# Kernel optimization log

Hardware: AMD Instinct MI355X
Metric: run time of the kernel (lower is better)

## Reference

```python
import jax, jax.numpy as jnp
import numpy as np
import math

NUM_HEADS = 2


def setup_inputs() -> dict:
    key = jax.random.key(0)
    k1, k2, k3, k4 = jax.random.split(key, 4)
    B, S, E = 16, 2048, 8  # embed_dim == n_wires == 8 (required by module structure)
    x = jax.random.normal(k1, (B, S, E), dtype=jnp.float32)
    theta = jax.random.normal(k2, (E,), dtype=jnp.float32)          # trainable RX angles, one per wire
    w_out = jax.random.normal(k3, (E, E), dtype=jnp.float32) / math.sqrt(E)  # out_proj weight
    b_out = jax.random.normal(k4, (E,), dtype=jnp.float32) * 0.01   # out_proj bias
    return {"x": x, "theta": theta, "w_out": w_out, "b_out": b_out}


def reference(x, theta, w_out, b_out):
    B, S, E = x.shape
    H = NUM_HEADS
    dk = E // H
    # Quantum projection, analytic form: per-wire RX(x) then RX(theta) on |0>,
    # PauliZ expectation -> cos(x + theta). Same layer applied for q, k, v.
    q = jnp.cos(x + theta)              # [B, S, E]
    qh = q.reshape(B, S, H, dk).transpose(0, 2, 1, 3)  # [B, H, S, dk]; q == k == v
    scores = jnp.einsum('bhqd,bhkd->bhqk', qh, qh) / jnp.sqrt(jnp.float32(dk))
    attn = jax.nn.softmax(scores, axis=-1)             # dropout is identity in eval
    out = jnp.einsum('bhqk,bhkd->bhqd', attn, qh)      # [B, H, S, dk]
    out = out.transpose(0, 2, 1, 3).reshape(B, S, E)
    return out @ w_out.T + b_out
```

## Files before the change

### kernel.cpp

```cpp
#include <hip/hip_runtime.h>
#include <math.h>

#define BB 16
#define SS 2048
#define HH 2
#define ROWS_PER_BLOCK 128
#define ROWS_PER_WAVE 32
#define THREADS1 256
#define NIH 2
#define KEYS_HALF (SS / NIH)
#define KT 16
#define NITER (KEYS_HALF / KT)
#define KVT_STRIDE 1040

typedef _Float16 half8 __attribute__((ext_vector_type(8)));
typedef _Float16 half4h __attribute__((ext_vector_type(4)));
typedef float floatx4 __attribute__((ext_vector_type(4)));

__device__ __forceinline__ float fast_exp2(float x) {
  return __builtin_amdgcn_exp2f(x);
}

__global__ __launch_bounds__(THREADS1, 4)
void qattn_mfma(const float* __restrict__ x,
                const float* __restrict__ theta,
                float* __restrict__ ws) {
  __shared__ half8 s_keys[KEYS_HALF];
  __shared__ _Float16 s_kvT[5 * KVT_STRIDE];
  __shared__ half4h s_rows[ROWS_PER_BLOCK];

  const int bid = blockIdx.x;
  const int rb  = bid & 15;
  const int bh  = (bid >> 4) & 31;
  const int ih  = bid >> 9;
  const int b   = bh >> 1;
  const int h   = bh & 1;
  const int t   = threadIdx.x;

  const float4 th = ((const float4*)theta)[h];
  const float4* xb = (const float4*)x;

  for (int i = t; i < KEYS_HALF; i += THREADS1) {
    const int s = ih * KEYS_HALF + i;
    float4 xr = xb[(size_t)(b * SS + s) * 2 + h];
    _Float16 c0 = (_Float16)__cosf(xr.x + th.x);
    _Float16 c1 = (_Float16)__cosf(xr.y + th.y);
    _Float16 c2 = (_Float16)__cosf(xr.z + th.z);
    _Float16 c3 = (_Float16)__cosf(xr.w + th.w);
    const _Float16 z = (_Float16)0.0f;
    half8 v = {c0, c1, c2, c3, z, z, z, z};
    s_keys[i] = v;
    s_kvT[0 * KVT_STRIDE + i] = c0;
    s_kvT[1 * KVT_STRIDE + i] = c1;
    s_kvT[2 * KVT_STRIDE + i] = c2;
    s_kvT[3 * KVT_STRIDE + i] = c3;
  }
  for (int i = t; i < KVT_STRIDE; i += THREADS1)
    s_kvT[4 * KVT_STRIDE + i] = (_Float16)1.0f;
  for (int i = t; i < ROWS_PER_BLOCK; i += THREADS1) {
    const int s = rb * ROWS_PER_BLOCK + i;
    float4 xr = xb[(size_t)(b * SS + s) * 2 + h];
    half4h v = {(_Float16)__cosf(xr.x + th.x), (_Float16)__cosf(xr.y + th.y),
                (_Float16)__cosf(xr.z + th.z), (_Float16)__cosf(xr.w + th.w)};
    s_rows[i] = v;
  }
  __syncthreads();

  const int lane = t & 63;
  const int wv   = t >> 6;
  const int quad = lane >> 4;
  const int l15  = lane & 15;

  const float KS  = 0.72134752044448170367f;
  const float scl = (lane < 16) ? KS : 0.0f;
  half4h r0 = s_rows[wv * ROWS_PER_WAVE + l15];
  half4h r1 = s_rows[wv * ROWS_PER_WAVE + 16 + l15];
  const _Float16 z = (_Float16)0.0f;
  half8 b0 = {(_Float16)((float)r0[0] * scl), (_Float16)((float)r0[1] * scl),
              (_Float16)((float)r0[2] * scl), (_Float16)((float)r0[3] * scl), z, z, z, z};
  half8 b1 = {(_Float16)((float)r1[0] * scl), (_Float16)((float)r1[1] * scl),
              (_Float16)((float)r1[2] * scl), (_Float16)((float)r1[3] * scl), z, z, z, z};

  const _Float16* bpv_base =
      s_kvT + (l15 < 4 ? l15 : 4) * KVT_STRIDE + quad * 4;

  floatx4 o0 = {0.f, 0.f, 0.f, 0.f};
  floatx4 o1 = {0.f, 0.f, 0.f, 0.f};
  const floatx4 zf = {0.f, 0.f, 0.f, 0.f};
  half8 apv0 = {z, z, z, z, z, z, z, z};
  half8 apv1 = {z, z, z, z, z, z, z, z};

#pragma unroll 2
  for (int it = 0; it < NITER; ++it) {
    half8 a = s_keys[it * KT + l15];
    half4h bl = *(const half4h*)(bpv_base + it * KT);
    half8 bpv = {bl[0], bl[1], bl[2], bl[3], z, z, z, z};

    floatx4 c0 = __builtin_amdgcn_mfma_f32_16x16x32_f16(a, b0, zf, 0, 0, 0);
    floatx4 c1 = __builtin_amdgcn_mfma_f32_16x16x32_f16(a, b1, zf, 0, 0, 0);

    apv0[0] = (_Float16)fast_exp2(c0[0]);
    apv0[1] = (_Float16)fast_exp2(c0[1]);
    apv0[2] = (_Float16)fast_exp2(c0[2]);
    apv0[3] = (_Float16)fast_exp2(c0[3]);
    apv1[0] = (_Float16)fast_exp2(c1[0]);
    apv1[1] = (_Float16)fast_exp2(c1[1]);
    apv1[2] = (_Float16)fast_exp2(c1[2]);
    apv1[3] = (_Float16)fast_exp2(c1[3]);

    o0 = __builtin_amdgcn_mfma_f32_16x16x32_f16(apv0, bpv, o0, 0, 0, 0);
    o1 = __builtin_amdgcn_mfma_f32_16x16x32_f16(apv1, bpv, o1, 0, 0, 0);
  }

  if (l15 < 5) {
    const size_t base =
        ((size_t)(ih * 32 + bh) * SS + rb * ROWS_PER_BLOCK + wv * ROWS_PER_WAVE) * 8;
    float* w0 = ws + base + (size_t)(quad * 4) * 8 + l15;
    float* w1 = ws + base + (size_t)(16 + quad * 4) * 8 + l15;
    w0[0]  = o0[0]; w0[8]  = o0[1]; w0[16] = o0[2]; w0[24] = o0[3];
    w1[0]  = o1[0]; w1[8]  = o1[1]; w1[16] = o1[2]; w1[24] = o1[3];
  }
}

__global__ __launch_bounds__(256)
void qattn_proj(const float* __restrict__ ws,
                const float* __restrict__ w_out,
                const float* __restrict__ b_out,
                float* __restrict__ out) {
  const int gid = blockIdx.x * 256 + threadIdx.x;
  const int b = gid >> 11;
  const int s = gid & 2047;
  float o[8];
#pragma unroll
  for (int h = 0; h < HH; ++h) {
    const int bh = b * 2 + h;
    const size_t i0 = ((size_t)(0 * 32 + bh) * SS + s) * 8;
    const size_t i1 = ((size_t)(1 * 32 + bh) * SS + s) * 8;
    float4 A  = *(const float4*)(ws + i0);
    float  la = ws[i0 + 4];
    float4 Bv = *(const float4*)(ws + i1);
    float  lb = ws[i1 + 4];
    const float inv = 1.0f / (la + lb);
    o[h * 4 + 0] = (A.x + Bv.x) * inv;
    o[h * 4 + 1] = (A.y + Bv.y) * inv;
    o[h * 4 + 2] = (A.z + Bv.z) * inv;
    o[h * 4 + 3] = (A.w + Bv.w) * inv;
  }
  float r[8];
#pragma unroll
  for (int e = 0; e < 8; ++e) {
    float acc = b_out[e];
#pragma unroll
    for (int j = 0; j < 8; ++j) acc = fmaf(o[j], w_out[e * 8 + j], acc);
    r[e] = acc;
  }
  float* op = out + (size_t)gid * 8;
  *(float4*)op = make_float4(r[0], r[1], r[2], r[3]);
  *(float4*)(op + 4) = make_float4(r[4], r[5], r[6], r[7]);
}

extern "C" void kernel_launch(void* const* d_in, const int* in_sizes, int n_in,
                              void* d_out, int out_size, void* d_ws, size_t ws_size,
                              hipStream_t stream) {
  const float* x     = (const float*)d_in[0];
  const float* theta = (const float*)d_in[1];
  const float* w_out = (const float*)d_in[2];
  const float* b_out = (const float*)d_in[3];
  float* out = (float*)d_out;
  (void)in_sizes; (void)n_in; (void)out_size; (void)ws_size;

  qattn_mfma<<<dim3(NIH * 32 * 16), THREADS1, 0, stream>>>(x, theta, (float*)d_ws);
  qattn_proj<<<dim3((BB * SS) / 256), 256, 0, stream>>>((const float*)d_ws, w_out, b_out, out);
}
```

Before: 80.55 us.

## Fuse attention and output projection into one kernel with atomic head accumulation

Replaces the split-key attention kernel plus separate projection kernel with one fused kernel. Each block now covers all 2048 keys for one head and 128 query rows, using 8 waves of 16 rows each. It normalizes in shared memory and atomically adds each head's partial projection into the output, which is zeroed by a memset. The goal is to drop the workspace round trip and the second launch. In exchange it adds a memset, float atomics, more LDS per block and half as many blocks.

Measured after the change: 80.15 us. Within noise of the previous version (-0.5%).

```diff
diff --git a/kernel.cpp b/kernel.cpp
--- a/kernel.cpp
+++ b/kernel.cpp
@@ -5,43 +5,52 @@
 #define SS 2048
 #define HH 2
 #define ROWS_PER_BLOCK 128
-#define ROWS_PER_WAVE 32
-#define THREADS1 256
-#define NIH 2
-#define KEYS_HALF (SS / NIH)
+#define THREADS1 512
 #define KT 16
-#define NITER (KEYS_HALF / KT)
-#define KVT_STRIDE 1040
+#define NITER (SS / KT)
+#define KVT_STRIDE 2064
 
 typedef _Float16 half8 __attribute__((ext_vector_type(8)));
 typedef _Float16 half4h __attribute__((ext_vector_type(4)));
+typedef _Float16 half2h __attribute__((ext_vector_type(2)));
 typedef float floatx4 __attribute__((ext_vector_type(4)));
 
 __device__ __forceinline__ float fast_exp2(float x) {
   return __builtin_amdgcn_exp2f(x);
 }
 
+__device__ __forceinline__ half2h pkrtz(float a, float b) {
+#if defined(__has_builtin)
+#if __has_builtin(__builtin_amdgcn_cvt_pkrtz)
+  return __builtin_bit_cast(half2h, __builtin_amdgcn_cvt_pkrtz(a, b));
+#else
+  half2h r; r[0] = (_Float16)a; r[1] = (_Float16)b; return r;
+#endif
+#else
+  half2h r; r[0] = (_Float16)a; r[1] = (_Float16)b; return r;
+#endif
+}
+
 __global__ __launch_bounds__(THREADS1, 4)
-void qattn_mfma(const float* __restrict__ x,
-                const float* __restrict__ theta,
-                float* __restrict__ ws) {
-  __shared__ half8 s_keys[KEYS_HALF];
+void qattn_fused(const float* __restrict__ x,
+                 const float* __restrict__ theta,
+                 const float* __restrict__ w_out,
+                 const float* __restrict__ b_out,
+                 float* __restrict__ out) {
+  __shared__ half8 s_keys[SS];
   __shared__ _Float16 s_kvT[5 * KVT_STRIDE];
-  __shared__ half4h s_rows[ROWS_PER_BLOCK];
+  __shared__ float po[ROWS_PER_BLOCK * 6];
 
   const int bid = blockIdx.x;
   const int rb  = bid & 15;
-  const int bh  = (bid >> 4) & 31;
-  const int ih  = bid >> 9;
-  const int b   = bh >> 1;
-  const int h   = bh & 1;
+  const int h   = (bid >> 4) & 1;
+  const int b   = bid >> 5;
   const int t   = threadIdx.x;
 
   const float4 th = ((const float4*)theta)[h];
   const float4* xb = (const float4*)x;
 
-  for (int i = t; i < KEYS_HALF; i += THREADS1) {
-    const int s = ih * KEYS_HALF + i;
+  for (int s = t; s < SS; s += THREADS1) {
     float4 xr = xb[(size_t)(b * SS + s) * 2 + h];
     _Float16 c0 = (_Float16)__cosf(xr.x + th.x);
     _Float16 c1 = (_Float16)__cosf(xr.y + th.y);
@@ -49,21 +58,14 @@
     _Float16 c3 = (_Float16)__cosf(xr.w + th.w);
     const _Float16 z = (_Float16)0.0f;
     half8 v = {c0, c1, c2, c3, z, z, z, z};
-    s_keys[i] = v;
-    s_kvT[0 * KVT_STRIDE + i] = c0;
-    s_kvT[1 * KVT_STRIDE + i] = c1;
-    s_kvT[2 * KVT_STRIDE + i] = c2;
-    s_kvT[3 * KVT_STRIDE + i] = c3;
+    s_keys[s] = v;
+    s_kvT[0 * KVT_STRIDE + s] = c0;
+    s_kvT[1 * KVT_STRIDE + s] = c1;
+    s_kvT[2 * KVT_STRIDE + s] = c2;
+    s_kvT[3 * KVT_STRIDE + s] = c3;
   }
   for (int i = t; i < KVT_STRIDE; i += THREADS1)
     s_kvT[4 * KVT_STRIDE + i] = (_Float16)1.0f;
-  for (int i = t; i < ROWS_PER_BLOCK; i += THREADS1) {
-    const int s = rb * ROWS_PER_BLOCK + i;
-    float4 xr = xb[(size_t)(b * SS + s) * 2 + h];
-    half4h v = {(_Float16)__cosf(xr.x + th.x), (_Float16)__cosf(xr.y + th.y),
-                (_Float16)__cosf(xr.z + th.z), (_Float16)__cosf(xr.w + th.w)};
-    s_rows[i] = v;
-  }
   __syncthreads();
 
   const int lane = t & 63;
@@ -73,90 +75,58 @@
 
   const float KS  = 0.72134752044448170367f;
   const float scl = (lane < 16) ? KS : 0.0f;
-  half4h r0 = s_rows[wv * ROWS_PER_WAVE + l15];
-  half4h r1 = s_rows[wv * ROWS_PER_WAVE + 16 + l15];
+  const int   qrow = rb * ROWS_PER_BLOCK + wv * 16 + l15;
+  half4h rq = *(const half4h*)&s_keys[qrow];
   const _Float16 z = (_Float16)0.0f;
-  half8 b0 = {(_Float16)((float)r0[0] * scl), (_Float16)((float)r0[1] * scl),
-              (_Float16)((float)r0[2] * scl), (_Float16)((float)r0[3] * scl), z, z, z, z};
-  half8 b1 = {(_Float16)((float)r1[0] * scl), (_Float16)((float)r1[1] * scl),
-              (_Float16)((float)r1[2] * scl), (_Float16)((float)r1[3] * scl), z, z, z, z};
+  half8 bq = {(_Float16)((float)rq[0] * scl), (_Float16)((float)rq[1] * scl),
+              (_Float16)((float)rq[2] * scl), (_Float16)((float)rq[3] * scl),
+              z, z, z, z};
 
-  const _Float16* bpv_base =
-      s_kvT + (l15 < 4 ? l15 : 4) * KVT_STRIDE + quad * 4;
+  const _Float16* bbase = s_kvT + (l15 < 4 ? l15 : 4) * KVT_STRIDE + quad * 4;
 
-  floatx4 o0 = {0.f, 0.f, 0.f, 0.f};
-  floatx4 o1 = {0.f, 0.f, 0.f, 0.f};
+  floatx4 o = {0.f, 0.f, 0.f, 0.f};
   const floatx4 zf = {0.f, 0.f, 0.f, 0.f};
-  half8 apv0 = {z, z, z, z, z, z, z, z};
-  half8 apv1 = {z, z, z, z, z, z, z, z};
+  half8 apv = {z, z, z, z, z, z, z, z};
 
-#pragma unroll 2
-  for (int it = 0; it < NITER; ++it) {
-    half8 a = s_keys[it * KT + l15];
-    half4h bl = *(const half4h*)(bpv_base + it * KT);
+#pragma unroll 4
+  for (int kt = 0; kt < NITER; ++kt) {
+    half8 a = s_keys[kt * KT + l15];
+    half4h bl = *(const half4h*)(bbase + kt * KT);
     half8 bpv = {bl[0], bl[1], bl[2], bl[3], z, z, z, z};
 
-    floatx4 c0 = __builtin_amdgcn_mfma_f32_16x16x32_f16(a, b0, zf, 0, 0, 0);
-    floatx4 c1 = __builtin_amdgcn_mfma_f32_16x16x32_f16(a, b1, zf, 0, 0, 0);
+    floatx4 c = __builtin_amdgcn_mfma_f32_16x16x32_f16(a, bq, zf, 0, 0, 0);
 
-    apv0[0] = (_Float16)fast_exp2(c0[0]);
-    apv0[1] = (_Float16)fast_exp2(c0[1]);
-    apv0[2] = (_Float16)fast_exp2(c0[2]);
-    apv0[3] = (_Float16)fast_exp2(c0[3]);
-    apv1[0] = (_Float16)fast_exp2(c1[0]);
-    apv1[1] = (_Float16)fast_exp2(c1[1]);
-    apv1[2] = (_Float16)fast_exp2(c1[2]);
-    apv1[3] = (_Float16)fast_exp2(c1[3]);
+    half2h p01 = pkrtz(fast_exp2(c[0]), fast_exp2(c[1]));
+    half2h p23 = pkrtz(fast_exp2(c[2]), fast_exp2(c[3]));
+    apv[0] = p01[0]; apv[1] = p01[1]; apv[2] = p23[0]; apv[3] = p23[1];
 
-    o0 = __builtin_amdgcn_mfma_f32_16x16x32_f16(apv0, bpv, o0, 0, 0, 0);
-    o1 = __builtin_amdgcn_mfma_f32_16x16x32_f16(apv1, bpv, o1, 0, 0, 0);
+    o = __builtin_amdgcn_mfma_f32_16x16x32_f16(apv, bpv, o, 0, 0, 0);
   }
 
   if (l15 < 5) {
-    const size_t base =
-        ((size_t)(ih * 32 + bh) * SS + rb * ROWS_PER_BLOCK + wv * ROWS_PER_WAVE) * 8;
-    float* w0 = ws + base + (size_t)(quad * 4) * 8 + l15;
-    float* w1 = ws + base + (size_t)(16 + quad * 4) * 8 + l15;
-    w0[0]  = o0[0]; w0[8]  = o0[1]; w0[16] = o0[2]; w0[24] = o0[3];
-    w1[0]  = o1[0]; w1[8]  = o1[1]; w1[16] = o1[2]; w1[24] = o1[3];
+#pragma unroll
+    for (int r = 0; r < 4; ++r)
+      po[(wv * 16 + quad * 4 + r) * 6 + l15] = o[r];
   }
-}
+  __syncthreads();
 
-__global__ __launch_bounds__(256)
-void qattn_proj(const float* __restrict__ ws,
-                const float* __restrict__ w_out,
-                const float* __restrict__ b_out,
-                float* __restrict__ out) {
-  const int gid = blockIdx.x * 256 + threadIdx.x;
-  const int b = gid >> 11;
-  const int s = gid & 2047;
-  float o[8];
+  {
+    const int row = t >> 2;
+    const int ep  = (t & 3) * 2;
+    const float* pr = po + row * 6;
+    const float inv = 1.0f / pr[4];
+    const float o0 = pr[0] * inv, o1 = pr[1] * inv,
+                o2 = pr[2] * inv, o3 = pr[3] * inv;
+    float* op = out + ((size_t)(b * SS + rb * ROWS_PER_BLOCK + row)) * 8;
 #pragma unroll
-  for (int h = 0; h < HH; ++h) {
-    const int bh = b * 2 + h;
-    const size_t i0 = ((size_t)(0 * 32 + bh) * SS + s) * 8;
-    const size_t i1 = ((size_t)(1 * 32 + bh) * SS + s) * 8;
-    float4 A  = *(const float4*)(ws + i0);
-    float  la = ws[i0 + 4];
-    float4 Bv = *(const float4*)(ws + i1);
-    float  lb = ws[i1 + 4];
-    const float inv = 1.0f / (la + lb);
-    o[h * 4 + 0] = (A.x + Bv.x) * inv;
-    o[h * 4 + 1] = (A.y + Bv.y) * inv;
-    o[h * 4 + 2] = (A.z + Bv.z) * inv;
-    o[h * 4 + 3] = (A.w + Bv.w) * inv;
+    for (int k = 0; k < 2; ++k) {
+      const int e = ep + k;
+      const float* wr = w_out + e * 8 + h * 4;
+      float val = fmaf(o0, wr[0], fmaf(o1, wr[1], fmaf(o2, wr[2], o3 * wr[3])));
+      if (h == 0) val += b_out[e];
+      atomicAdd(op + e, val);
+    }
   }
-  float r[8];
-#pragma unroll
-  for (int e = 0; e < 8; ++e) {
-    float acc = b_out[e];
-#pragma unroll
-    for (int j = 0; j < 8; ++j) acc = fmaf(o[j], w_out[e * 8 + j], acc);
-    r[e] = acc;
-  }
-  float* op = out + (size_t)gid * 8;
-  *(float4*)op = make_float4(r[0], r[1], r[2], r[3]);
-  *(float4*)(op + 4) = make_float4(r[4], r[5], r[6], r[7]);
 }
 
 extern "C" void kernel_launch(void* const* d_in, const int* in_sizes, int n_in,
@@ -167,8 +137,8 @@
   const float* w_out = (const float*)d_in[2];
   const float* b_out = (const float*)d_in[3];
   float* out = (float*)d_out;
-  (void)in_sizes; (void)n_in; (void)out_size; (void)ws_size;
+  (void)in_sizes; (void)n_in; (void)d_ws; (void)ws_size;
 
-  qattn_mfma<<<dim3(NIH * 32 * 16), THREADS1, 0, stream>>>(x, theta, (float*)d_ws);
-  qattn_proj<<<dim3((BB * SS) / 256), 256, 0, stream>>>((const float*)d_ws, w_out, b_out, out);
+  (void)hipMemsetAsync(d_out, 0, (size_t)out_size * sizeof(float), stream);
+  qattn_fused<<<dim3(BB * HH * 16), THREADS1, 0, stream>>>(x, theta, w_out, b_out, out);
 }
```

## Use 32x32x16 MFMA tiles and split keys eight ways across blocks

Applied to the files above, without the earlier changes.

Replaces the paired 16x16x32 MFMAs with a single 32x32x16 score MFMA per 32-key tile. The exponentials are packed with cvt_pkrtz and fed to two 32x32 PV MFMAs. The key split grows from 2 to 8 chunks, which quadruples the grid and shrinks shared memory per block, allowing higher occupancy (launch bounds 8). The cost is a larger partial-sum workspace that the merge kernel must read and reduce, plus an index permutation on the transposed V storage.

After: 83.16 us. 1.03x slower.

```diff
diff --git a/kernel.cpp b/kernel.cpp
--- a/kernel.cpp
+++ b/kernel.cpp
@@ -4,30 +4,30 @@
 #define BB 16
 #define SS 2048
 #define HH 2
-#define ROWS_PER_BLOCK 128
-#define ROWS_PER_WAVE 32
-#define THREADS1 256
-#define NIH 2
-#define KEYS_HALF (SS / NIH)
-#define KT 16
-#define NITER (KEYS_HALF / KT)
-#define KVT_STRIDE 1040
+#define NIH 8
+#define KCHUNK (SS / NIH)
+#define RPB 128
+#define THREADS 256
+#define NITER (KCHUNK / 32)
+#define KVT_STRIDE 264
 
 typedef _Float16 half8 __attribute__((ext_vector_type(8)));
-typedef _Float16 half4h __attribute__((ext_vector_type(4)));
-typedef float floatx4 __attribute__((ext_vector_type(4)));
+typedef _Float16 half2h __attribute__((ext_vector_type(2)));
+typedef float floatx16 __attribute__((ext_vector_type(16)));
 
 __device__ __forceinline__ float fast_exp2(float x) {
   return __builtin_amdgcn_exp2f(x);
 }
+__device__ __forceinline__ half2h pkrtz(float a, float b) {
+  return __builtin_bit_cast(half2h, __builtin_amdgcn_cvt_pkrtz(a, b));
+}
 
-__global__ __launch_bounds__(THREADS1, 4)
-void qattn_mfma(const float* __restrict__ x,
+__global__ __launch_bounds__(THREADS, 8)
+void qattn_part(const float* __restrict__ x,
                 const float* __restrict__ theta,
                 float* __restrict__ ws) {
-  __shared__ half8 s_keys[KEYS_HALF];
+  __shared__ half8 s_keys[KCHUNK];
   __shared__ _Float16 s_kvT[5 * KVT_STRIDE];
-  __shared__ half4h s_rows[ROWS_PER_BLOCK];
 
   const int bid = blockIdx.x;
   const int rb  = bid & 15;
@@ -38,95 +38,85 @@
   const int t   = threadIdx.x;
 
   const float4 th = ((const float4*)theta)[h];
-  const float4* xb = (const float4*)x;
+  const float4* x4 = (const float4*)x;
 
-  for (int i = t; i < KEYS_HALF; i += THREADS1) {
-    const int s = ih * KEYS_HALF + i;
-    float4 xr = xb[(size_t)(b * SS + s) * 2 + h];
-    _Float16 c0 = (_Float16)__cosf(xr.x + th.x);
-    _Float16 c1 = (_Float16)__cosf(xr.y + th.y);
-    _Float16 c2 = (_Float16)__cosf(xr.z + th.z);
-    _Float16 c3 = (_Float16)__cosf(xr.w + th.w);
+  {
+    const int s = ih * KCHUNK + t;
+    float4 xr = x4[(size_t)(b * SS + s) * 2 + h];
+    float c0 = __cosf(xr.x + th.x), c1 = __cosf(xr.y + th.y);
+    float c2 = __cosf(xr.z + th.z), c3 = __cosf(xr.w + th.w);
     const _Float16 z = (_Float16)0.0f;
-    half8 v = {c0, c1, c2, c3, z, z, z, z};
-    s_keys[i] = v;
-    s_kvT[0 * KVT_STRIDE + i] = c0;
-    s_kvT[1 * KVT_STRIDE + i] = c1;
-    s_kvT[2 * KVT_STRIDE + i] = c2;
-    s_kvT[3 * KVT_STRIDE + i] = c3;
+    half8 v = {(_Float16)c0, (_Float16)c1, (_Float16)c2, (_Float16)c3, z, z, z, z};
+    s_keys[t] = v;
+    const int q = t & 15;
+    const int pos = (t & ~15) | ((q & 3) | ((q & 4) << 1) | ((q & 8) >> 1));
+    s_kvT[0 * KVT_STRIDE + pos] = (_Float16)c0;
+    s_kvT[1 * KVT_STRIDE + pos] = (_Float16)c1;
+    s_kvT[2 * KVT_STRIDE + pos] = (_Float16)c2;
+    s_kvT[3 * KVT_STRIDE + pos] = (_Float16)c3;
   }
-  for (int i = t; i < KVT_STRIDE; i += THREADS1)
+  for (int i = t; i < KVT_STRIDE; i += THREADS)
     s_kvT[4 * KVT_STRIDE + i] = (_Float16)1.0f;
-  for (int i = t; i < ROWS_PER_BLOCK; i += THREADS1) {
-    const int s = rb * ROWS_PER_BLOCK + i;
-    float4 xr = xb[(size_t)(b * SS + s) * 2 + h];
-    half4h v = {(_Float16)__cosf(xr.x + th.x), (_Float16)__cosf(xr.y + th.y),
-                (_Float16)__cosf(xr.z + th.z), (_Float16)__cosf(xr.w + th.w)};
-    s_rows[i] = v;
-  }
-  __syncthreads();
 
   const int lane = t & 63;
   const int wv   = t >> 6;
-  const int quad = lane >> 4;
-  const int l15  = lane & 15;
+  const int g    = lane >> 5;
+  const int n    = lane & 31;
+  const int row  = rb * RPB + wv * 32 + n;
 
   const float KS  = 0.72134752044448170367f;
-  const float scl = (lane < 16) ? KS : 0.0f;
-  half4h r0 = s_rows[wv * ROWS_PER_WAVE + l15];
-  half4h r1 = s_rows[wv * ROWS_PER_WAVE + 16 + l15];
+  const float scl = g ? 0.0f : KS;
+  float4 xq = x4[(size_t)(b * SS + row) * 2 + h];
   const _Float16 z = (_Float16)0.0f;
-  half8 b0 = {(_Float16)((float)r0[0] * scl), (_Float16)((float)r0[1] * scl),
-              (_Float16)((float)r0[2] * scl), (_Float16)((float)r0[3] * scl), z, z, z, z};
-  half8 b1 = {(_Float16)((float)r1[0] * scl), (_Float16)((float)r1[1] * scl),
-              (_Float16)((float)r1[2] * scl), (_Float16)((float)r1[3] * scl), z, z, z, z};
+  half8 bq = {(_Float16)(__cosf(xq.x + th.x) * scl),
+              (_Float16)(__cosf(xq.y + th.y) * scl),
+              (_Float16)(__cosf(xq.z + th.z) * scl),
+              (_Float16)(__cosf(xq.w + th.w) * scl), z, z, z, z};
+  __syncthreads();
 
-  const _Float16* bpv_base =
-      s_kvT + (l15 < 4 ? l15 : 4) * KVT_STRIDE + quad * 4;
+  const _Float16* bb = s_kvT + (n < 4 ? n : 4) * KVT_STRIDE + 8 * g;
 
-  floatx4 o0 = {0.f, 0.f, 0.f, 0.f};
-  floatx4 o1 = {0.f, 0.f, 0.f, 0.f};
-  const floatx4 zf = {0.f, 0.f, 0.f, 0.f};
-  half8 apv0 = {z, z, z, z, z, z, z, z};
-  half8 apv1 = {z, z, z, z, z, z, z, z};
+  floatx16 o  = {0,0,0,0,0,0,0,0,0,0,0,0,0,0,0,0};
+  const floatx16 zf = {0,0,0,0,0,0,0,0,0,0,0,0,0,0,0,0};
 
-#pragma unroll 2
-  for (int it = 0; it < NITER; ++it) {
-    half8 a = s_keys[it * KT + l15];
-    half4h bl = *(const half4h*)(bpv_base + it * KT);
-    half8 bpv = {bl[0], bl[1], bl[2], bl[3], z, z, z, z};
+#pragma unroll
+  for (int kt = 0; kt < NITER; ++kt) {
+    half8 a  = s_keys[kt * 32 + n];
+    half8 b1 = *(const half8*)(bb + kt * 32);
+    half8 b2 = *(const half8*)(bb + kt * 32 + 16);
 
-    floatx4 c0 = __builtin_amdgcn_mfma_f32_16x16x32_f16(a, b0, zf, 0, 0, 0);
-    floatx4 c1 = __builtin_amdgcn_mfma_f32_16x16x32_f16(a, b1, zf, 0, 0, 0);
+    floatx16 c = __builtin_amdgcn_mfma_f32_32x32x16_f16(a, bq, zf, 0, 0, 0);
 
-    apv0[0] = (_Float16)fast_exp2(c0[0]);
-    apv0[1] = (_Float16)fast_exp2(c0[1]);
-    apv0[2] = (_Float16)fast_exp2(c0[2]);
-    apv0[3] = (_Float16)fast_exp2(c0[3]);
-    apv1[0] = (_Float16)fast_exp2(c1[0]);
-    apv1[1] = (_Float16)fast_exp2(c1[1]);
-    apv1[2] = (_Float16)fast_exp2(c1[2]);
-    apv1[3] = (_Float16)fast_exp2(c1[3]);
+    half2h p0 = pkrtz(fast_exp2(c[0]),  fast_exp2(c[1]));
+    half2h p1 = pkrtz(fast_exp2(c[2]),  fast_exp2(c[3]));
+    half2h p2 = pkrtz(fast_exp2(c[4]),  fast_exp2(c[5]));
+    half2h p3 = pkrtz(fast_exp2(c[6]),  fast_exp2(c[7]));
+    half2h p4 = pkrtz(fast_exp2(c[8]),  fast_exp2(c[9]));
+    half2h p5 = pkrtz(fast_exp2(c[10]), fast_exp2(c[11]));
+    half2h p6 = pkrtz(fast_exp2(c[12]), fast_exp2(c[13]));
+    half2h p7 = pkrtz(fast_exp2(c[14]), fast_exp2(c[15]));
+    half8 pa1 = {p0[0], p0[1], p1[0], p1[1], p2[0], p2[1], p3[0], p3[1]};
+    half8 pa2 = {p4[0], p4[1], p5[0], p5[1], p6[0], p6[1], p7[0], p7[1]};
 
-    o0 = __builtin_amdgcn_mfma_f32_16x16x32_f16(apv0, bpv, o0, 0, 0, 0);
-    o1 = __builtin_amdgcn_mfma_f32_16x16x32_f16(apv1, bpv, o1, 0, 0, 0);
+    o = __builtin_amdgcn_mfma_f32_32x32x16_f16(pa1, b1, o, 0, 0, 0);
+    o = __builtin_amdgcn_mfma_f32_32x32x16_f16(pa2, b2, o, 0, 0, 0);
   }
 
-  if (l15 < 5) {
-    const size_t base =
-        ((size_t)(ih * 32 + bh) * SS + rb * ROWS_PER_BLOCK + wv * ROWS_PER_WAVE) * 8;
-    float* w0 = ws + base + (size_t)(quad * 4) * 8 + l15;
-    float* w1 = ws + base + (size_t)(16 + quad * 4) * 8 + l15;
-    w0[0]  = o0[0]; w0[8]  = o0[1]; w0[16] = o0[2]; w0[24] = o0[3];
-    w1[0]  = o1[0]; w1[8]  = o1[1]; w1[16] = o1[2]; w1[24] = o1[3];
+  if (n < 5) {
+    float* wp = ws + ((size_t)(ih * 32 + bh) * SS + rb * RPB + wv * 32 + 4 * g) * 8 + n;
+#pragma unroll
+    for (int r = 0; r < 16; ++r) {
+      const int m = (r & 3) + 8 * (r >> 2);
+      wp[(size_t)m * 8] = o[r];
+    }
   }
 }
 
 __global__ __launch_bounds__(256)
-void qattn_proj(const float* __restrict__ ws,
-                const float* __restrict__ w_out,
-                const float* __restrict__ b_out,
-                float* __restrict__ out) {
+void qattn_merge(const float* __restrict__ ws,
+                 const float* __restrict__ w_out,
+                 const float* __restrict__ b_out,
+                 float* __restrict__ out) {
   const int gid = blockIdx.x * 256 + threadIdx.x;
   const int b = gid >> 11;
   const int s = gid & 2047;
@@ -134,17 +124,20 @@
 #pragma unroll
   for (int h = 0; h < HH; ++h) {
     const int bh = b * 2 + h;
-    const size_t i0 = ((size_t)(0 * 32 + bh) * SS + s) * 8;
-    const size_t i1 = ((size_t)(1 * 32 + bh) * SS + s) * 8;
-    float4 A  = *(const float4*)(ws + i0);
-    float  la = ws[i0 + 4];
-    float4 Bv = *(const float4*)(ws + i1);
-    float  lb = ws[i1 + 4];
-    const float inv = 1.0f / (la + lb);
-    o[h * 4 + 0] = (A.x + Bv.x) * inv;
-    o[h * 4 + 1] = (A.y + Bv.y) * inv;
-    o[h * 4 + 2] = (A.z + Bv.z) * inv;
-    o[h * 4 + 3] = (A.w + Bv.w) * inv;
+    float4 acc = make_float4(0.f, 0.f, 0.f, 0.f);
+    float l = 0.f;
+#pragma unroll
+    for (int ih = 0; ih < NIH; ++ih) {
+      const size_t idx = ((size_t)(ih * 32 + bh) * SS + s) * 8;
+      float4 a = *(const float4*)(ws + idx);
+      acc.x += a.x; acc.y += a.y; acc.z += a.z; acc.w += a.w;
+      l += ws[idx + 4];
+    }
+    const float inv = 1.0f / l;
+    o[h * 4 + 0] = acc.x * inv;
+    o[h * 4 + 1] = acc.y * inv;
+    o[h * 4 + 2] = acc.z * inv;
+    o[h * 4 + 3] = acc.w * inv;
   }
   float r[8];
 #pragma unroll
@@ -155,7 +148,7 @@
     r[e] = acc;
   }
   float* op = out + (size_t)gid * 8;
-  *(float4*)op = make_float4(r[0], r[1], r[2], r[3]);
+  *(float4*)op       = make_float4(r[0], r[1], r[2], r[3]);
   *(float4*)(op + 4) = make_float4(r[4], r[5], r[6], r[7]);
 }
 
@@ -169,6 +162,6 @@
   float* out = (float*)d_out;
   (void)in_sizes; (void)n_in; (void)out_size; (void)ws_size;
 
-  qattn_mfma<<<dim3(NIH * 32 * 16), THREADS1, 0, stream>>>(x, theta, (float*)d_ws);
-  qattn_proj<<<dim3((BB * SS) / 256), 256, 0, stream>>>((const float*)d_ws, w_out, b_out, out);
+  qattn_part<<<dim3(NIH * 32 * 16), THREADS, 0, stream>>>(x, theta, (float*)d_ws);
+  qattn_merge<<<dim3((BB * SS) / 256), 256, 0, stream>>>((const float*)d_ws, w_out, b_out, out);
 }
```
